# Kernel optimization log

Hardware: AMD Instinct MI355X
Metric: run time of the kernel (lower is better)

## Reference

```python
import jax, jax.numpy as jnp
import numpy as np

HIDDEN = 64

def setup_inputs() -> dict:
    key = jax.random.key(0)
    ks = jax.random.split(key, 8)
    B, T, D, O, H = 1024, 256, 128, 128, HIDDEN
    s_ih = 1.0 / np.sqrt(H)
    inp = {
        "x": jax.random.normal(ks[0], (B, T, D), dtype=jnp.float32),
        "W_ih": jax.random.uniform(ks[1], (4 * H, D), jnp.float32, -s_ih, s_ih),
        "W_hh": jax.random.uniform(ks[2], (4 * H, H), jnp.float32, -s_ih, s_ih),
        "b_ih": jax.random.uniform(ks[3], (4 * H,), jnp.float32, -s_ih, s_ih),
        "b_hh": jax.random.uniform(ks[4], (4 * H,), jnp.float32, -s_ih, s_ih),
        "W_o": jax.random.uniform(ks[5], (O, H), jnp.float32, -s_ih, s_ih),
        "b_o": jax.random.uniform(ks[6], (O,), jnp.float32, -s_ih, s_ih),
    }
    return inp

def _lstm_last_h(x, W_ih, W_hh, b_ih, b_hh):
    # x: [B, T, D]. PyTorch gate order: i, f, g, o.
    B, T, D = x.shape
    H = HIDDEN
    # Precompute input contribution for all steps: [T, B, 4H]
    gx = jnp.einsum('btd,gd->tbg', x, W_ih) + (b_ih + b_hh)

    def step(carry, gx_t):
        h, c = carry
        gates = gx_t + h @ W_hh.T  # [B, 4H]
        i = jax.nn.sigmoid(gates[:, 0 * H:1 * H])
        f = jax.nn.sigmoid(gates[:, 1 * H:2 * H])
        g = jnp.tanh(gates[:, 2 * H:3 * H])
        o = jax.nn.sigmoid(gates[:, 3 * H:4 * H])
        c = f * c + i * g
        h = o * jnp.tanh(c)
        return (h, c), None

    h0 = jnp.zeros((B, H), x.dtype)
    c0 = jnp.zeros((B, H), x.dtype)
    (h_T, _), _ = jax.lax.scan(step, (h0, c0), gx)
    return h_T  # [B, H] == output[:, -1, :]

def reference(x, W_ih, W_hh, b_ih, b_hh, W_o, b_o):
    h = _lstm_last_h(x, W_ih, W_hh, b_ih, b_hh)
    logits = jax.nn.relu(h) @ W_o.T + b_o  # [B, O]; dropout is identity in eval
    return jax.nn.log_softmax(logits, axis=1)
```

## Files before the change

### kernel.cpp

```cpp
#include <hip/hip_runtime.h>
#include <math.h>

constexpr int B = 1024, T = 256, D = 128, H = 64, O = 128;
constexpr int BQ = 4;
constexpr int NBLK = B / BQ;
constexpr int FT = 4;
constexpr int NF = T / FT;
constexpr int NBUF = 4;
constexpr int JP = 20;
constexpr int TSP = 64 * JP + 4;
constexpr int BUFSZ = FT * TSP;

typedef __attribute__((ext_vector_type(8))) short short8;
typedef __attribute__((ext_vector_type(4))) float f32x4;

__device__ __forceinline__ unsigned short f2bf(float f) {
    union { float f; unsigned u; } v; v.f = f;
    return (unsigned short)((v.u + 0x7FFF + ((v.u >> 16) & 1)) >> 16);
}
__device__ __forceinline__ float frcp(float x) { return __builtin_amdgcn_rcpf(x); }
__device__ __forceinline__ float sigmoidf_(float x) {
    return frcp(1.0f + __expf(-x));
}
__device__ __forceinline__ float tanhf_(float x) {
    return fmaf(2.0f, frcp(1.0f + __expf(-2.0f * x)), -1.0f);
}

template<int T0, int NT>
__device__ __forceinline__ void producer_loop(
    const float* __restrict__ x, const float* __restrict__ Wih,
    const float* __restrict__ bih, const float* __restrict__ bhh,
    float* gxb, volatile int* vfree, int* fillcnt, int b0, int lane)
{
    const int lq = lane & 15;
    const int qd = lane >> 4;

    short8 wf[NT][4];
    float  bs[NT];
    #pragma unroll
    for (int ti = 0; ti < NT; ++ti) {
        const int G = 16 * (T0 + ti) + lq;
        #pragma unroll
        for (int c = 0; c < 4; ++c) {
            const float* p = Wih + (size_t)G * D + 32 * c + 8 * qd;
            short8 v;
            #pragma unroll
            for (int j = 0; j < 8; ++j) v[j] = (short)f2bf(p[j]);
            wf[ti][c] = v;
        }
        bs[ti] = bih[G] + bhh[G];
    }

    const float* xb = x + ((size_t)(b0 + (lq & 3)) * T + (lq >> 2)) * D + 8 * qd;
    float4 pf[4][2];
    auto iload = [&](int f) {
        #pragma unroll
        for (int c = 0; c < 4; ++c) {
            const float* p = xb + (size_t)(FT * f) * D + 32 * c;
            pf[c][0] = *(const float4*)p;
            pf[c][1] = *(const float4*)(p + 4);
        }
    };
    iload(0);

    for (int f = 0; f < NF; ++f) {
        short8 xf[4];
        #pragma unroll
        for (int c = 0; c < 4; ++c) {
            float4 a = pf[c][0], bv = pf[c][1];
            short8 v;
            v[0] = (short)f2bf(a.x);  v[1] = (short)f2bf(a.y);
            v[2] = (short)f2bf(a.z);  v[3] = (short)f2bf(a.w);
            v[4] = (short)f2bf(bv.x); v[5] = (short)f2bf(bv.y);
            v[6] = (short)f2bf(bv.z); v[7] = (short)f2bf(bv.w);
            xf[c] = v;
        }
        if (f + 1 < NF) iload(f + 1);

        const int epoch = f >> 2;
        while (vfree[f & 3] < epoch) __builtin_amdgcn_s_sleep(2);

        float* buf = gxb + (f & 3) * BUFSZ + qd * TSP + lq * JP;
        #pragma unroll
        for (int ti = 0; ti < NT; ++ti) {
            const int t = T0 + ti;
            f32x4 a = {bs[ti], bs[ti], bs[ti], bs[ti]};
            #pragma unroll
            for (int c = 0; c < 4; ++c)
                a = __builtin_amdgcn_mfma_f32_16x16x32_bf16(xf[c], wf[ti][c], a, 0, 0, 0);
            float* wp = buf + (16 * (t & 3)) * JP + (t >> 2);
            #pragma unroll
            for (int r = 0; r < 4; ++r) wp[4 * r] = a[r];
        }
        asm volatile("s_waitcnt lgkmcnt(0)" ::: "memory");
        atomicAdd(&fillcnt[f & 3], 1);
    }
}

__global__ __launch_bounds__(256, 1)
void lstm_fused(const float* __restrict__ x, const float* __restrict__ Wih,
                const float* __restrict__ Whh, const float* __restrict__ bih,
                const float* __restrict__ bhh, const float* __restrict__ Wo,
                const float* __restrict__ bo, float* __restrict__ out)
{
    __shared__ float gxb[NBUF * BUFSZ];
    __shared__ unsigned short hlds[4 * 80];
    __shared__ float hfin[4 * 64];
    __shared__ int fillcnt[NBUF];
    __shared__ int freecnt[NBUF];

    const int tid  = threadIdx.x;
    const int lane = tid & 63;
    const int w    = tid >> 6;
    const int lq   = lane & 15;
    const int qd   = lane >> 4;
    const int b0   = blockIdx.x * BQ;

    if (tid < NBUF) { fillcnt[tid] = 0; freecnt[tid] = 0; }
    if (tid < 160) ((unsigned int*)hlds)[tid] = 0u;
    __syncthreads();

    if (w == 3) {
        short8 whh_f[16][2];
        #pragma unroll
        for (int t = 0; t < 16; ++t)
            #pragma unroll
            for (int c = 0; c < 2; ++c) {
                const float* p = Whh + (size_t)(16 * t + lq) * H + 32 * c + 8 * qd;
                short8 v;
                #pragma unroll
                for (int j = 0; j < 8; ++j) v[j] = (short)f2bf(p[j]);
                whh_f[t][c] = v;
            }

        const char* hbase = (const char*)hlds + (lq >> 2) * 160 + 16 * qd;

        volatile int* vfill = fillcnt;
        f32x4 gxn[4];
        auto wait_fill = [&](int f) {
            const int tgt = 3 * ((f >> 2) + 1);
            while (vfill[f & 3] < tgt) __builtin_amdgcn_s_sleep(2);
        };
        auto pre = [&](int tt) {
            const float* p = gxb + ((tt >> 2) & 3) * BUFSZ + (tt & 3) * TSP +
                             lq * JP + 4 * qd;
            #pragma unroll
            for (int s = 0; s < 4; ++s)
                gxn[s] = *(const f32x4*)(p + s * 16 * JP);
        };

        wait_fill(0);
        pre(0);

        float cst[4] = {0.f, 0.f, 0.f, 0.f};
        float hv4[4];

        for (int tt = 0; tt < T; ++tt) {
            short8 h0 = *(const short8*)hbase;
            short8 h1 = *(const short8*)(hbase + 64);

            #pragma unroll
            for (int s = 0; s < 4; ++s) {
                f32x4 a0 = {0.f,0.f,0.f,0.f}, a1 = a0, a2 = a0, a3 = a0;
                a0 = __builtin_amdgcn_mfma_f32_16x16x32_bf16(h0, whh_f[s][0], a0, 0,0,0);
                a0 = __builtin_amdgcn_mfma_f32_16x16x32_bf16(h1, whh_f[s][1], a0, 0,0,0);
                a1 = __builtin_amdgcn_mfma_f32_16x16x32_bf16(h0, whh_f[4+s][0], a1, 0,0,0);
                a1 = __builtin_amdgcn_mfma_f32_16x16x32_bf16(h1, whh_f[4+s][1], a1, 0,0,0);
                a2 = __builtin_amdgcn_mfma_f32_16x16x32_bf16(h0, whh_f[8+s][0], a2, 0,0,0);
                a2 = __builtin_amdgcn_mfma_f32_16x16x32_bf16(h1, whh_f[8+s][1], a2, 0,0,0);
                a3 = __builtin_amdgcn_mfma_f32_16x16x32_bf16(h0, whh_f[12+s][0], a3, 0,0,0);
                a3 = __builtin_amdgcn_mfma_f32_16x16x32_bf16(h1, whh_f[12+s][1], a3, 0,0,0);

                float gi = sigmoidf_(a0[0] + gxn[s][0]);
                float gf = sigmoidf_(a1[0] + gxn[s][1]);
                float gg = tanhf_  (a2[0] + gxn[s][2]);
                float go = sigmoidf_(a3[0] + gxn[s][3]);
                cst[s] = fmaf(gf, cst[s], gi * gg);
                float hv = go * tanhf_(cst[s]);
                hv4[s] = hv;
                hlds[qd * 80 + 16 * s + lq] = f2bf(hv);
            }

            if ((tt & 3) == 3) {
                asm volatile("s_waitcnt lgkmcnt(0)" ::: "memory");
                atomicAdd(&freecnt[(tt >> 2) & 3], 1);
                if (tt + 1 < T) wait_fill((tt + 1) >> 2);
            }
            if (tt + 1 < T) pre(tt + 1);
        }

        #pragma unroll
        for (int s = 0; s < 4; ++s)
            hfin[qd * 64 + 16 * s + lq] = hv4[s];
    } else if (w == 0) {
        producer_loop<0, 6>(x, Wih, bih, bhh, gxb, freecnt, fillcnt, b0, lane);
    } else if (w == 1) {
        producer_loop<6, 5>(x, Wih, bih, bhh, gxb, freecnt, fillcnt, b0, lane);
    } else {
        producer_loop<11, 5>(x, Wih, bih, bhh, gxb, freecnt, fillcnt, b0, lane);
    }

    __syncthreads();

    {
        const int m = w;
        float l0 = bo[lane], l1 = bo[lane + 64];
        const float* w0 = Wo + (size_t)lane * H;
        const float* w1 = Wo + (size_t)(lane + 64) * H;
        #pragma unroll
        for (int k = 0; k < H; ++k) {
            float rh = fmaxf(hfin[m * 64 + k], 0.0f);
            l0 = fmaf(rh, w0[k], l0);
            l1 = fmaf(rh, w1[k], l1);
        }
        float mx = fmaxf(l0, l1);
        #pragma unroll
        for (int sh = 32; sh > 0; sh >>= 1) mx = fmaxf(mx, __shfl_xor(mx, sh));
        float e = __expf(l0 - mx) + __expf(l1 - mx);
        #pragma unroll
        for (int sh = 32; sh > 0; sh >>= 1) e += __shfl_xor(e, sh);
        float lse = mx + __logf(e);
        float* op = out + (size_t)(b0 + m) * O;
        op[lane]      = l0 - lse;
        op[lane + 64] = l1 - lse;
    }
}

extern "C" void kernel_launch(void* const* d_in, const int* in_sizes, int n_in,
                              void* d_out, int out_size, void* d_ws, size_t ws_size,
                              hipStream_t stream) {
    const float* x   = (const float*)d_in[0];
    const float* Wih = (const float*)d_in[1];
    const float* Whh = (const float*)d_in[2];
    const float* bih = (const float*)d_in[3];
    const float* bhh = (const float*)d_in[4];
    const float* Wo  = (const float*)d_in[5];
    const float* bo  = (const float*)d_in[6];
    lstm_fused<<<dim3(NBLK), dim3(256), 0, stream>>>(
        x, Wih, Whh, bih, bhh, Wo, bo, (float*)d_out);
}
```

Baseline: 331.7 us.

## Split LSTM recurrence across two consumer waves with double-buffered hidden state

```diff
diff --git a/kernel.cpp b/kernel.cpp
--- a/kernel.cpp
+++ b/kernel.cpp
@@ -78,7 +78,7 @@
         if (f + 1 < NF) iload(f + 1);
 
         const int epoch = f >> 2;
-        while (vfree[f & 3] < epoch) __builtin_amdgcn_s_sleep(2);
+        while (vfree[f & 3] < 2 * epoch) __builtin_amdgcn_s_sleep(2);
 
         float* buf = gxb + (f & 3) * BUFSZ + qd * TSP + lq * JP;
         #pragma unroll
@@ -104,10 +104,11 @@
                 const float* __restrict__ bo, float* __restrict__ out)
 {
     __shared__ float gxb[NBUF * BUFSZ];
-    __shared__ unsigned short hlds[4 * 80];
+    __shared__ unsigned short hlds[2 * 320];
     __shared__ float hfin[4 * 64];
     __shared__ int fillcnt[NBUF];
     __shared__ int freecnt[NBUF];
+    __shared__ int cseq[2];
 
     const int tid  = threadIdx.x;
     const int lane = tid & 63;
@@ -117,89 +118,101 @@
     const int b0   = blockIdx.x * BQ;
 
     if (tid < NBUF) { fillcnt[tid] = 0; freecnt[tid] = 0; }
+    if (tid < 2) cseq[tid] = 0;
     if (tid < 160) ((unsigned int*)hlds)[tid] = 0u;
     __syncthreads();
 
-    if (w == 3) {
-        short8 whh_f[16][2];
-        #pragma unroll
-        for (int t = 0; t < 16; ++t)
-            #pragma unroll
-            for (int c = 0; c < 2; ++c) {
-                const float* p = Whh + (size_t)(16 * t + lq) * H + 32 * c + 8 * qd;
-                short8 v;
+    float hv[2] = {0.f, 0.f};
+    int   cwg = -1;
+
+    if (w >= 2) {
+        const int cw = w - 2;   cwg = cw;
+        short8 whh_f[4][2][2];
+        #pragma unroll
+        for (int q = 0; q < 4; ++q)
+            #pragma unroll
+            for (int si = 0; si < 2; ++si)
                 #pragma unroll
-                for (int j = 0; j < 8; ++j) v[j] = (short)f2bf(p[j]);
-                whh_f[t][c] = v;
-            }
-
-        const char* hbase = (const char*)hlds + (lq >> 2) * 160 + 16 * qd;
+                for (int c = 0; c < 2; ++c) {
+                    const int G = 64 * q + 32 * cw + 16 * si + lq;
+                    const float* p = Whh + (size_t)G * H + 32 * c + 8 * qd;
+                    short8 v;
+                    #pragma unroll
+                    for (int j = 0; j < 8; ++j) v[j] = (short)f2bf(p[j]);
+                    whh_f[q][si][c] = v;
+                }
 
         volatile int* vfill = fillcnt;
-        f32x4 gxn[4];
+        volatile int* vseq  = cseq;
+        f32x4 gxn[2];
         auto wait_fill = [&](int f) {
-            const int tgt = 3 * ((f >> 2) + 1);
+            const int tgt = 2 * ((f >> 2) + 1);
             while (vfill[f & 3] < tgt) __builtin_amdgcn_s_sleep(2);
         };
         auto pre = [&](int tt) {
-            const float* p = gxb + ((tt >> 2) & 3) * BUFSZ + (tt & 3) * TSP +
-                             lq * JP + 4 * qd;
-            #pragma unroll
-            for (int s = 0; s < 4; ++s)
-                gxn[s] = *(const f32x4*)(p + s * 16 * JP);
+            const float* p = gxb + ((tt >> 2) & 3) * BUFSZ + (tt & 3) * TSP + 4 * qd;
+            gxn[0] = *(const f32x4*)(p + (16 * (2 * cw + 0) + lq) * JP);
+            gxn[1] = *(const f32x4*)(p + (16 * (2 * cw + 1) + lq) * JP);
         };
 
         wait_fill(0);
         pre(0);
 
-        float cst[4] = {0.f, 0.f, 0.f, 0.f};
-        float hv4[4];
+        float cst[2] = {0.f, 0.f};
+        const int hb = (lq >> 2) * 80 + 8 * qd;
 
         for (int tt = 0; tt < T; ++tt) {
-            short8 h0 = *(const short8*)hbase;
-            short8 h1 = *(const short8*)(hbase + 64);
-
-            #pragma unroll
-            for (int s = 0; s < 4; ++s) {
-                f32x4 a0 = {0.f,0.f,0.f,0.f}, a1 = a0, a2 = a0, a3 = a0;
-                a0 = __builtin_amdgcn_mfma_f32_16x16x32_bf16(h0, whh_f[s][0], a0, 0,0,0);
-                a0 = __builtin_amdgcn_mfma_f32_16x16x32_bf16(h1, whh_f[s][1], a0, 0,0,0);
-                a1 = __builtin_amdgcn_mfma_f32_16x16x32_bf16(h0, whh_f[4+s][0], a1, 0,0,0);
-                a1 = __builtin_amdgcn_mfma_f32_16x16x32_bf16(h1, whh_f[4+s][1], a1, 0,0,0);
-                a2 = __builtin_amdgcn_mfma_f32_16x16x32_bf16(h0, whh_f[8+s][0], a2, 0,0,0);
-                a2 = __builtin_amdgcn_mfma_f32_16x16x32_bf16(h1, whh_f[8+s][1], a2, 0,0,0);
-                a3 = __builtin_amdgcn_mfma_f32_16x16x32_bf16(h0, whh_f[12+s][0], a3, 0,0,0);
-                a3 = __builtin_amdgcn_mfma_f32_16x16x32_bf16(h1, whh_f[12+s][1], a3, 0,0,0);
-
-                float gi = sigmoidf_(a0[0] + gxn[s][0]);
-                float gf = sigmoidf_(a1[0] + gxn[s][1]);
-                float gg = tanhf_  (a2[0] + gxn[s][2]);
-                float go = sigmoidf_(a3[0] + gxn[s][3]);
-                cst[s] = fmaf(gf, cst[s], gi * gg);
-                float hv = go * tanhf_(cst[s]);
-                hv4[s] = hv;
-                hlds[qd * 80 + 16 * s + lq] = f2bf(hv);
+            const unsigned short* hc = hlds + (tt & 1) * 320;
+            short8 h0 = *(const short8*)(hc + hb);
+            short8 h1 = *(const short8*)(hc + hb + 32);
+
+            f32x4 acc[4][2];
+            #pragma unroll
+            for (int q = 0; q < 4; ++q)
+                #pragma unroll
+                for (int si = 0; si < 2; ++si) {
+                    const float g = gxn[si][q];
+                    f32x4 a = {g, g, g, g};
+                    a = __builtin_amdgcn_mfma_f32_16x16x32_bf16(h0, whh_f[q][si][0], a, 0, 0, 0);
+                    a = __builtin_amdgcn_mfma_f32_16x16x32_bf16(h1, whh_f[q][si][1], a, 0, 0, 0);
+                    acc[q][si] = a;
+                }
+
+            unsigned short* hn = hlds + ((tt + 1) & 1) * 320;
+            #pragma unroll
+            for (int si = 0; si < 2; ++si) {
+                float gi = sigmoidf_(acc[0][si][0]);
+                float gf = sigmoidf_(acc[1][si][0]);
+                float gg = tanhf_  (acc[2][si][0]);
+                float go = sigmoidf_(acc[3][si][0]);
+                cst[si] = fmaf(gf, cst[si], gi * gg);
+                hv[si]  = go * tanhf_(cst[si]);
+                hn[qd * 80 + 16 * (2 * cw + si) + lq] = f2bf(hv[si]);
             }
 
+            asm volatile("s_waitcnt lgkmcnt(0)" ::: "memory");
+            if (lane == 0) ((volatile int*)cseq)[cw] = tt + 1;
+
             if ((tt & 3) == 3) {
-                asm volatile("s_waitcnt lgkmcnt(0)" ::: "memory");
                 atomicAdd(&freecnt[(tt >> 2) & 3], 1);
                 if (tt + 1 < T) wait_fill((tt + 1) >> 2);
             }
             if (tt + 1 < T) pre(tt + 1);
-        }
-
-        #pragma unroll
-        for (int s = 0; s < 4; ++s)
-            hfin[qd * 64 + 16 * s + lq] = hv4[s];
+
+            while (vseq[1 - cw] < tt + 1) {}
+            asm volatile("" ::: "memory");
+        }
     } else if (w == 0) {
-        producer_loop<0, 6>(x, Wih, bih, bhh, gxb, freecnt, fillcnt, b0, lane);
-    } else if (w == 1) {
-        producer_loop<6, 5>(x, Wih, bih, bhh, gxb, freecnt, fillcnt, b0, lane);
+        producer_loop<0, 8>(x, Wih, bih, bhh, gxb, freecnt, fillcnt, b0, lane);
     } else {
-        producer_loop<11, 5>(x, Wih, bih, bhh, gxb, freecnt, fillcnt, b0, lane);
-    }
-
+        producer_loop<8, 8>(x, Wih, bih, bhh, gxb, freecnt, fillcnt, b0, lane);
+    }
+
+    if (cwg >= 0) {
+        #pragma unroll
+        for (int si = 0; si < 2; ++si)
+            hfin[qd * 64 + 16 * (2 * cwg + si) + lq] = hv[si];
+    }
     __syncthreads();
 
     {
```

Result: faster. 302.4 us (-8.9%).
